# Performance work log

Measured on AMD Instinct MI355X. Metric: run time of the kernel, lower is better.

## Reference

```python
import jax, jax.numpy as jnp
import numpy as np
from jax import lax

VOCAB, NUM_CLASSES = 21128, 53
EMB, FILT, K = 128, 128, 3
B, L = 512, 512


def setup_inputs() -> dict:
    key = jax.random.key(0)
    ks = jax.random.split(key, 8)
    char_ids = jax.random.randint(ks[0], (B, L), 0, VOCAB, dtype=jnp.int64 if jax.config.jax_enable_x64 else jnp.int32)
    pos_e1 = jax.random.randint(ks[1], (B,), 0, L - 1, dtype=jnp.int32)
    pos_e2 = jax.random.randint(ks[2], (B,), 0, L - 1, dtype=jnp.int32)
    emb_table = jax.random.normal(ks[3], (VOCAB, EMB), dtype=jnp.float32) * 0.02
    emb_table = emb_table.at[0].set(0.0)  # padding_idx=0
    conv_w = jax.random.normal(ks[4], (FILT, EMB, K), dtype=jnp.float32) * (1.0 / np.sqrt(EMB * K))
    conv_b = jax.random.normal(ks[5], (FILT,), dtype=jnp.float32) * 0.01
    fc_w = jax.random.normal(ks[6], (NUM_CLASSES, FILT * 3), dtype=jnp.float32) * (1.0 / np.sqrt(FILT * 3))
    fc_b = jax.random.normal(ks[7], (NUM_CLASSES,), dtype=jnp.float32) * 0.01
    return {"char_ids": char_ids, "pos_e1": pos_e1, "pos_e2": pos_e2,
            "emb_table": emb_table, "conv_w": conv_w, "conv_b": conv_b,
            "fc_w": fc_w, "fc_b": fc_b}


def reference(char_ids, pos_e1, pos_e2, emb_table, conv_w, conv_b, fc_w, fc_b):
    b, seq = char_ids.shape
    x = emb_table[char_ids]                      # (b, L, E)
    x = jnp.transpose(x, (0, 2, 1))              # (b, E, L)
    conv_out = lax.conv_general_dilated(
        x, conv_w, window_strides=(1,), padding=[(K // 2, K // 2)],
        dimension_numbers=("NCH", "OIH", "NCH"))
    conv_out = jax.nn.relu(conv_out + conv_b[None, :, None])  # (b, F, L)

    # sort + clip entity boundaries, replicate e1==e2 -> e2=e1+1 adjustment
    e1 = jnp.clip(jnp.minimum(pos_e1, pos_e2), 0, seq)
    e2 = jnp.clip(jnp.maximum(pos_e1, pos_e2), 0, seq)
    e2 = jnp.where(e1 == e2, jnp.minimum(e1 + 1, seq), e2)

    idx = jnp.arange(seq)[None, :]               # (1, L)
    m1 = idx < jnp.maximum(e1, 1)[:, None]       # [:e1] or [:1] if e1==0
    m2 = (idx >= e1[:, None]) & (idx < e2[:, None])
    m3 = idx >= jnp.minimum(e2, seq - 1)[:, None]  # [e2:] or last col if e2==L

    neg = jnp.float32(-jnp.inf)
    def seg_max(mask):
        return jnp.max(jnp.where(mask[:, None, :], conv_out, neg), axis=-1)  # (b, F)

    pooled = jnp.concatenate([seg_max(m1), seg_max(m2), seg_max(m3)], axis=-1)  # (b, 3F)
    return pooled @ fc_w.T + fc_b
```

## Files before the change

### kernel.cpp

```cpp
#include <hip/hip_runtime.h>
#include <stdint.h>

#define VOCAB 21128
#define NUMC  53
#define EMB   128
#define SEQ   512
#define BATCH 512

typedef __bf16 bf16x8 __attribute__((ext_vector_type(8)));
typedef float f32x4 __attribute__((ext_vector_type(4)));

__device__ __forceinline__ unsigned int f2bf1(float f) {
    union { float f; unsigned int u; } v; v.f = f;
    return (v.u + 0x7FFFu + ((v.u >> 16) & 1u)) >> 16;
}
__device__ __forceinline__ unsigned int pack2(float a, float b) {
    return f2bf1(a) | (f2bf1(b) << 16);
}

__global__ void prep_kernel(const float* __restrict__ emb, const float* __restrict__ cw,
                            unsigned short* __restrict__ Tb, unsigned short* __restrict__ Wp) {
    int idx = blockIdx.x * blockDim.x + threadIdx.x;
    const int n8 = VOCAB * EMB / 8;
    if (idx < n8) {
        const float4* src = (const float4*)emb + (size_t)idx * 2;
        float4 a = src[0], b = src[1];
        uint4 o;
        o.x = pack2(a.x, a.y);
        o.y = pack2(a.z, a.w);
        o.z = pack2(b.x, b.y);
        o.w = pack2(b.z, b.w);
        *(uint4*)(Tb + (size_t)idx * 8) = o;
    }
    if (idx < 12 * 8 * 64 * 8) {
        int j = idx & 7, l = (idx >> 3) & 63, g = (idx >> 9) & 7, s = idx >> 12;
        int kk = s * 32 + (l >> 4) * 8 + j;
        int f = g * 16 + (l & 15);
        int tap = kk >> 7, e = kk & 127;
        Wp[idx] = (unsigned short)f2bf1(cw[(f * EMB + e) * 3 + tap]);
    }
}

__launch_bounds__(512, 2)
__global__ void pcnn_main(const int* __restrict__ cid, const int* __restrict__ p1,
                          const int* __restrict__ p2,
                          const unsigned short* __restrict__ Tb,
                          const unsigned short* __restrict__ Wp,
                          const float* __restrict__ cb, const float* __restrict__ fcw,
                          const float* __restrict__ fcb, float* __restrict__ out) {
    __shared__ __align__(16) unsigned short xs[2][130 * 136];
    __shared__ unsigned int sid[514];
    __shared__ float pstage[2][3][128];
    __shared__ float pooled[384];
    __shared__ float fcred[NUMC][4];

    const int b    = blockIdx.x;
    const int tid  = threadIdx.x;
    const int lane = tid & 63;
    const int w    = tid >> 6;
    const int wm   = w & 1;
    const int wn   = w >> 1;
    const int quad = lane >> 4;
    const int lc   = lane & 15;

    for (int i = tid; i < 514; i += 512) {
        int gp = i - 1;
        unsigned int id = (gp >= 0 && gp < SEQ) ? (unsigned int)cid[(size_t)b * SEQ + gp] : 0u;
        sid[i] = id * 256u;
    }

    bf16x8 bfr[12][2];
#pragma unroll
    for (int s = 0; s < 12; ++s)
#pragma unroll
        for (int nt = 0; nt < 2; ++nt) {
            int g = wn * 2 + nt;
            bfr[s][nt] = *(const bf16x8*)(Wp + (size_t)((s * 8 + g) * 64 + lane) * 8);
        }

    int e1 = min(p1[b], p2[b]);
    int e2 = max(p1[b], p2[b]);
    if (e1 == e2) e2 = min(e1 + 1, SEQ);
    const int e1m = max(e1, 1);

    float smax[3][2];
#pragma unroll
    for (int s3 = 0; s3 < 3; ++s3) { smax[s3][0] = -1e30f; smax[s3][1] = -1e30f; }

    const char* TbB = (const char*)Tb;
    const int cc = tid & 15;
    const int r0 = tid >> 4;

    __syncthreads();

    uint4 g[5];
#pragma unroll
    for (int i = 0; i < 5; ++i) {
        int r = r0 + 32 * i;
        if (r < 130) g[i] = *(const uint4*)(TbB + sid[r] + cc * 16);
    }
#pragma unroll
    for (int i = 0; i < 5; ++i) {
        int r = r0 + 32 * i;
        if (r < 130) *(uint4*)(&xs[0][r * 136 + cc * 8]) = g[i];
    }

    for (int t = 0; t < 4; ++t) {
        __syncthreads();

        if (t < 3) {
#pragma unroll
            for (int i = 0; i < 5; ++i) {
                int r = r0 + 32 * i;
                if (r < 130) g[i] = *(const uint4*)(TbB + sid[(t + 1) * 128 + r] + cc * 16);
            }
        }

        const unsigned short* xb = xs[t & 1];
        f32x4 acc[4][2];
#pragma unroll
        for (int mt = 0; mt < 4; ++mt)
#pragma unroll
            for (int nt = 0; nt < 2; ++nt)
                acc[mt][nt] = (f32x4){0.f, 0.f, 0.f, 0.f};

#pragma unroll
        for (int s = 0; s < 12; ++s) {
            const int tap = s >> 2;
            const int eb  = (s & 3) * 32;
            bf16x8 af[4];
#pragma unroll
            for (int mt = 0; mt < 4; ++mt) {
                int r = wm * 64 + mt * 16 + lc + tap;
                af[mt] = *(const bf16x8*)(xb + r * 136 + eb + quad * 8);
            }
#pragma unroll
            for (int mt = 0; mt < 4; ++mt)
#pragma unroll
                for (int nt = 0; nt < 2; ++nt)
                    acc[mt][nt] = __builtin_amdgcn_mfma_f32_16x16x32_bf16(
                        af[mt], bfr[s][nt], acc[mt][nt], 0, 0, 0);
        }

#pragma unroll
        for (int mt = 0; mt < 4; ++mt)
#pragma unroll
            for (int reg = 0; reg < 4; ++reg) {
                int p = t * 128 + wm * 64 + mt * 16 + quad * 4 + reg;
                float a0 = (p < e1m) ? 0.f : -2e30f;
                float a1 = (p >= e1 && p < e2) ? 0.f : -2e30f;
                float a2 = (p >= e2) ? 0.f : -2e30f;
#pragma unroll
                for (int nt = 0; nt < 2; ++nt) {
                    float v = acc[mt][nt][reg];
                    smax[0][nt] = fmaxf(smax[0][nt], v + a0);
                    smax[1][nt] = fmaxf(smax[1][nt], v + a1);
                    smax[2][nt] = fmaxf(smax[2][nt], v + a2);
                }
            }

        if (t < 3) {
#pragma unroll
            for (int i = 0; i < 5; ++i) {
                int r = r0 + 32 * i;
                if (r < 130) *(uint4*)(&xs[(t + 1) & 1][r * 136 + cc * 8]) = g[i];
            }
        }
    }

#pragma unroll
    for (int s3 = 0; s3 < 3; ++s3)
#pragma unroll
        for (int nt = 0; nt < 2; ++nt) {
            float v = smax[s3][nt];
            v = fmaxf(v, __shfl_xor(v, 16));
            v = fmaxf(v, __shfl_xor(v, 32));
            smax[s3][nt] = v;
        }
    if (lane < 16) {
#pragma unroll
        for (int s3 = 0; s3 < 3; ++s3)
#pragma unroll
            for (int nt = 0; nt < 2; ++nt)
                pstage[wm][s3][(wn * 2 + nt) * 16 + lc] = smax[s3][nt];
    }
    __syncthreads();

    if (tid < 384) {
        int s3 = tid >> 7, f = tid & 127;
        float m = fmaxf(pstage[0][s3][f], pstage[1][s3][f]);
        pooled[tid] = fmaxf(m + cb[f], 0.f);
    }
    __syncthreads();

    if (tid < 212) {
        int c = tid >> 2, q = tid & 3;
        const float* wrow = fcw + (size_t)c * 384 + q * 96;
        const float* pp   = pooled + q * 96;
        float sum = 0.f;
#pragma unroll 8
        for (int i = 0; i < 96; ++i) sum += wrow[i] * pp[i];
        fcred[c][q] = sum;
    }
    __syncthreads();
    if (tid < NUMC)
        out[(size_t)b * NUMC + tid] =
            fcred[tid][0] + fcred[tid][1] + fcred[tid][2] + fcred[tid][3] + fcb[tid];
}

extern "C" void kernel_launch(void* const* d_in, const int* in_sizes, int n_in,
                              void* d_out, int out_size, void* d_ws, size_t ws_size,
                              hipStream_t stream) {
    const int*   cid = (const int*)d_in[0];
    const int*   p1  = (const int*)d_in[1];
    const int*   p2  = (const int*)d_in[2];
    const float* emb = (const float*)d_in[3];
    const float* cw  = (const float*)d_in[4];
    const float* cb  = (const float*)d_in[5];
    const float* fcw = (const float*)d_in[6];
    const float* fcb = (const float*)d_in[7];
    float* out = (float*)d_out;

    unsigned short* Tb = (unsigned short*)d_ws;
    unsigned short* Wp = (unsigned short*)((char*)d_ws + (size_t)VOCAB * EMB * 2);

    const int n8 = VOCAB * EMB / 8;
    const int prep_threads = 256;
    const int prep_blocks  = (n8 + prep_threads - 1) / prep_threads;
    prep_kernel<<<prep_blocks, prep_threads, 0, stream>>>(emb, cw, Tb, Wp);
    pcnn_main<<<BATCH, 512, 0, stream>>>(cid, p1, p2, Tb, Wp, cb, fcw, fcb, out);
}
```

Before: 127.5 us.

## Split each sequence into four tile blocks and combine pooled maxima separately

The single per-batch kernel, which looped over four 128-position tiles with double-buffered LDS, is replaced by a kernel launching one block per (batch, tile), so there are four times as many blocks. Each writes partial segment maxima to workspace. A new combine kernel reduces them and applies bias, ReLU and the FC layer. This raises parallelism and cuts LDS per block, at the cost of an extra launch, a global round trip for partials, and reloading conv weights in every block.

```diff
diff --git a/kernel.cpp b/kernel.cpp
--- a/kernel.cpp
+++ b/kernel.cpp
@@ -42,19 +42,17 @@
 }
 
 __launch_bounds__(512, 2)
-__global__ void pcnn_main(const int* __restrict__ cid, const int* __restrict__ p1,
+__global__ void pcnn_tile(const int* __restrict__ cid, const int* __restrict__ p1,
                           const int* __restrict__ p2,
                           const unsigned short* __restrict__ Tb,
                           const unsigned short* __restrict__ Wp,
-                          const float* __restrict__ cb, const float* __restrict__ fcw,
-                          const float* __restrict__ fcb, float* __restrict__ out) {
-    __shared__ __align__(16) unsigned short xs[2][130 * 136];
-    __shared__ unsigned int sid[514];
+                          float* __restrict__ Pd) {
+    __shared__ __align__(16) unsigned short xs[130 * 136];
     __shared__ float pstage[2][3][128];
-    __shared__ float pooled[384];
-    __shared__ float fcred[NUMC][4];
-
-    const int b    = blockIdx.x;
+
+    const int bx   = blockIdx.x;
+    const int b    = bx >> 2;
+    const int tq   = bx & 3;
     const int tid  = threadIdx.x;
     const int lane = tid & 63;
     const int w    = tid >> 6;
@@ -63,110 +61,80 @@
     const int quad = lane >> 4;
     const int lc   = lane & 15;
 
-    for (int i = tid; i < 514; i += 512) {
-        int gp = i - 1;
-        unsigned int id = (gp >= 0 && gp < SEQ) ? (unsigned int)cid[(size_t)b * SEQ + gp] : 0u;
-        sid[i] = id * 256u;
-    }
-
-    bf16x8 bfr[12][2];
-#pragma unroll
-    for (int s = 0; s < 12; ++s)
-#pragma unroll
-        for (int nt = 0; nt < 2; ++nt) {
-            int g = wn * 2 + nt;
-            bfr[s][nt] = *(const bf16x8*)(Wp + (size_t)((s * 8 + g) * 64 + lane) * 8);
-        }
+    const char* TbB = (const char*)Tb;
+    const int cc = tid & 15;
+    const int r0 = tid >> 4;
+    int ids[5];
+#pragma unroll
+    for (int i = 0; i < 5; ++i) {
+        int r = r0 + 32 * i;
+        int p = tq * 128 + r - 1;
+        ids[i] = (r < 130 && p >= 0 && p < SEQ) ? cid[(size_t)b * SEQ + p] : 0;
+    }
+    uint4 g[5];
+#pragma unroll
+    for (int i = 0; i < 5; ++i) {
+        int r = r0 + 32 * i;
+        if (r < 130) g[i] = *(const uint4*)(TbB + (size_t)(unsigned)ids[i] * 256u + cc * 16);
+    }
+#pragma unroll
+    for (int i = 0; i < 5; ++i) {
+        int r = r0 + 32 * i;
+        if (r < 130) *(uint4*)(&xs[r * 136 + cc * 8]) = g[i];
+    }
 
     int e1 = min(p1[b], p2[b]);
     int e2 = max(p1[b], p2[b]);
     if (e1 == e2) e2 = min(e1 + 1, SEQ);
     const int e1m = max(e1, 1);
 
+    __syncthreads();
+
+    f32x4 acc[4][2];
+#pragma unroll
+    for (int mt = 0; mt < 4; ++mt)
+#pragma unroll
+        for (int nt = 0; nt < 2; ++nt)
+            acc[mt][nt] = (f32x4){0.f, 0.f, 0.f, 0.f};
+
+#pragma unroll
+    for (int s = 0; s < 12; ++s) {
+        const int tap = s >> 2;
+        const int eb  = (s & 3) * 32;
+        bf16x8 b0 = *(const bf16x8*)(Wp + (size_t)((s * 8 + wn * 2) * 64 + lane) * 8);
+        bf16x8 b1 = *(const bf16x8*)(Wp + (size_t)((s * 8 + wn * 2 + 1) * 64 + lane) * 8);
+        bf16x8 af[4];
+#pragma unroll
+        for (int mt = 0; mt < 4; ++mt) {
+            int r = wm * 64 + mt * 16 + lc + tap;
+            af[mt] = *(const bf16x8*)(xs + r * 136 + eb + quad * 8);
+        }
+#pragma unroll
+        for (int mt = 0; mt < 4; ++mt) {
+            acc[mt][0] = __builtin_amdgcn_mfma_f32_16x16x32_bf16(af[mt], b0, acc[mt][0], 0, 0, 0);
+            acc[mt][1] = __builtin_amdgcn_mfma_f32_16x16x32_bf16(af[mt], b1, acc[mt][1], 0, 0, 0);
+        }
+    }
+
     float smax[3][2];
 #pragma unroll
     for (int s3 = 0; s3 < 3; ++s3) { smax[s3][0] = -1e30f; smax[s3][1] = -1e30f; }
-
-    const char* TbB = (const char*)Tb;
-    const int cc = tid & 15;
-    const int r0 = tid >> 4;
-
-    __syncthreads();
-
-    uint4 g[5];
-#pragma unroll
-    for (int i = 0; i < 5; ++i) {
-        int r = r0 + 32 * i;
-        if (r < 130) g[i] = *(const uint4*)(TbB + sid[r] + cc * 16);
-    }
-#pragma unroll
-    for (int i = 0; i < 5; ++i) {
-        int r = r0 + 32 * i;
-        if (r < 130) *(uint4*)(&xs[0][r * 136 + cc * 8]) = g[i];
-    }
-
-    for (int t = 0; t < 4; ++t) {
-        __syncthreads();
-
-        if (t < 3) {
-#pragma unroll
-            for (int i = 0; i < 5; ++i) {
-                int r = r0 + 32 * i;
-                if (r < 130) g[i] = *(const uint4*)(TbB + sid[(t + 1) * 128 + r] + cc * 16);
+#pragma unroll
+    for (int mt = 0; mt < 4; ++mt)
+#pragma unroll
+        for (int reg = 0; reg < 4; ++reg) {
+            int p = tq * 128 + wm * 64 + mt * 16 + quad * 4 + reg;
+            float a0 = (p < e1m) ? 0.f : -2e30f;
+            float a1 = (p >= e1 && p < e2) ? 0.f : -2e30f;
+            float a2 = (p >= e2) ? 0.f : -2e30f;
+#pragma unroll
+            for (int nt = 0; nt < 2; ++nt) {
+                float v = acc[mt][nt][reg];
+                smax[0][nt] = fmaxf(smax[0][nt], v + a0);
+                smax[1][nt] = fmaxf(smax[1][nt], v + a1);
+                smax[2][nt] = fmaxf(smax[2][nt], v + a2);
             }
         }
-
-        const unsigned short* xb = xs[t & 1];
-        f32x4 acc[4][2];
-#pragma unroll
-        for (int mt = 0; mt < 4; ++mt)
-#pragma unroll
-            for (int nt = 0; nt < 2; ++nt)
-                acc[mt][nt] = (f32x4){0.f, 0.f, 0.f, 0.f};
-
-#pragma unroll
-        for (int s = 0; s < 12; ++s) {
-            const int tap = s >> 2;
-            const int eb  = (s & 3) * 32;
-            bf16x8 af[4];
-#pragma unroll
-            for (int mt = 0; mt < 4; ++mt) {
-                int r = wm * 64 + mt * 16 + lc + tap;
-                af[mt] = *(const bf16x8*)(xb + r * 136 + eb + quad * 8);
-            }
-#pragma unroll
-            for (int mt = 0; mt < 4; ++mt)
-#pragma unroll
-                for (int nt = 0; nt < 2; ++nt)
-                    acc[mt][nt] = __builtin_amdgcn_mfma_f32_16x16x32_bf16(
-                        af[mt], bfr[s][nt], acc[mt][nt], 0, 0, 0);
-        }
-
-#pragma unroll
-        for (int mt = 0; mt < 4; ++mt)
-#pragma unroll
-            for (int reg = 0; reg < 4; ++reg) {
-                int p = t * 128 + wm * 64 + mt * 16 + quad * 4 + reg;
-                float a0 = (p < e1m) ? 0.f : -2e30f;
-                float a1 = (p >= e1 && p < e2) ? 0.f : -2e30f;
-                float a2 = (p >= e2) ? 0.f : -2e30f;
-#pragma unroll
-                for (int nt = 0; nt < 2; ++nt) {
-                    float v = acc[mt][nt][reg];
-                    smax[0][nt] = fmaxf(smax[0][nt], v + a0);
-                    smax[1][nt] = fmaxf(smax[1][nt], v + a1);
-                    smax[2][nt] = fmaxf(smax[2][nt], v + a2);
-                }
-            }
-
-        if (t < 3) {
-#pragma unroll
-            for (int i = 0; i < 5; ++i) {
-                int r = r0 + 32 * i;
-                if (r < 130) *(uint4*)(&xs[(t + 1) & 1][r * 136 + cc * 8]) = g[i];
-            }
-        }
-    }
 
 #pragma unroll
     for (int s3 = 0; s3 < 3; ++s3)
@@ -188,8 +156,23 @@
 
     if (tid < 384) {
         int s3 = tid >> 7, f = tid & 127;
-        float m = fmaxf(pstage[0][s3][f], pstage[1][s3][f]);
-        pooled[tid] = fmaxf(m + cb[f], 0.f);
+        Pd[((size_t)b * 4 + tq) * 384 + tid] = fmaxf(pstage[0][s3][f], pstage[1][s3][f]);
+    }
+}
+
+__launch_bounds__(256, 4)
+__global__ void pcnn_combine(const float* __restrict__ Pd, const float* __restrict__ cb,
+                             const float* __restrict__ fcw, const float* __restrict__ fcb,
+                             float* __restrict__ out) {
+    __shared__ float pooled[384];
+    __shared__ float fcred[NUMC][4];
+    const int b = blockIdx.x;
+    const int tid = threadIdx.x;
+
+    for (int j = tid; j < 384; j += 256) {
+        const float* pp = Pd + (size_t)b * 4 * 384 + j;
+        float m = fmaxf(fmaxf(pp[0], pp[384]), fmaxf(pp[768], pp[1152]));
+        pooled[j] = fmaxf(m + cb[j & 127], 0.f);
     }
     __syncthreads();
 
@@ -223,10 +206,12 @@
 
     unsigned short* Tb = (unsigned short*)d_ws;
     unsigned short* Wp = (unsigned short*)((char*)d_ws + (size_t)VOCAB * EMB * 2);
+    float*          Pd = (float*)((char*)d_ws + (size_t)VOCAB * EMB * 2 + 98304);
 
     const int n8 = VOCAB * EMB / 8;
     const int prep_threads = 256;
     const int prep_blocks  = (n8 + prep_threads - 1) / prep_threads;
     prep_kernel<<<prep_blocks, prep_threads, 0, stream>>>(emb, cw, Tb, Wp);
-    pcnn_main<<<BATCH, 512, 0, stream>>>(cid, p1, p2, Tb, Wp, cb, fcw, fcb, out);
-}
+    pcnn_tile<<<BATCH * 4, 512, 0, stream>>>(cid, p1, p2, Tb, Wp, Pd);
+    pcnn_combine<<<BATCH, 256, 0, stream>>>(Pd, cb, fcw, fcb, out);
+}
```

Result: slower. 130.7 us (+2.5%).
